# Kernel tuning notes

Measured on AMD Instinct MI355X. Metric: run time of the kernel, lower is better.

## Reference

```python
import jax, jax.numpy as jnp
import numpy as np

B, T, D = 4, 2048, 1024
H = int(D * 8.0)          # SwiGLU hidden (ffn_ratio=8)
SPARSITY = 0.95
THRESHOLD = 0.05          # PLIF firing threshold
PLIF_TAU = 2.5            # PLIF tau init
ALPHA = 2.0               # atan surrogate sharpness
EPS = 1e-6


@jax.custom_vjp
def spike(x):
    # Heaviside in fwd; atan surrogate gradient in bwd.
    return (x > 0).astype(x.dtype)

def _spike_fwd(x):
    return spike(x), x

def _spike_bwd(x, g):
    return (g * (ALPHA / 2.0) / (1.0 + (jnp.pi / 2.0 * ALPHA * x) ** 2),)

spike.defvjp(_spike_fwd, _spike_bwd)


def rmsnorm(x, w):
    return x * jax.lax.rsqrt(jnp.mean(x * x, axis=-1, keepdims=True) + EPS) * w


def setup_inputs() -> dict:
    key = jax.random.key(0)
    ks = jax.random.split(key, 12)
    f32 = jnp.float32
    return {
        "x": jax.random.normal(ks[0], (B, T, D), f32),
        "ln1_w": jnp.ones((D,), f32),
        "liq_win": (jax.random.normal(ks[1], (D, D), f32) / np.float32(np.sqrt(D))),
        "liq_wrec": (jax.random.normal(ks[2], (D, D), f32) / np.float32(np.sqrt(D))),
        "liq_b": jnp.zeros((D,), f32),
        "liq_tau": jnp.ones((D,), f32),  # softplus -> per-unit time constant
        "plif_w": jnp.asarray(-np.log(PLIF_TAU - 1.0), f32),  # sigmoid(w)=1/tau
        "syn_w": jax.random.normal(ks[3], (D, D), f32) * 0.02,
        "gate_w": jax.random.normal(ks[4], (D, D), f32) * 0.01,
        "gate_b": jnp.zeros((D,), f32),
        "ln2_w": jnp.ones((D,), f32),
        "ffn_wg": jax.random.normal(ks[5], (H, D), f32) * 0.02,
        "ffn_wu": jax.random.normal(ks[6], (H, D), f32) * 0.02,
        "ffn_wd": jax.random.normal(ks[7], (D, H), f32) * (0.02 / np.float32(np.sqrt(2.0))),
        "syn_mask": (jax.random.uniform(ks[8], (D, D)) > SPARSITY),  # bool, fixed
    }


def reference(x, ln1_w, liq_win, liq_wrec, liq_b, liq_tau, plif_w, syn_w,
              gate_w, gate_b, ln2_w, ffn_wg, ffn_wu, ffn_wd, syn_mask):
    # --- pre-norm ---
    a = rmsnorm(x, ln1_w)                       # (B,T,D)
    a_t = jnp.swapaxes(a, 0, 1)                 # (T,B,D)

    # --- LiquidCell: liquid time-constant recurrence over T ---
    tau = jax.nn.softplus(liq_tau)              # (D,) per-unit time constant

    def liq_step(h, xt):
        pre = xt @ liq_win.T + h @ liq_wrec.T + liq_b
        h = h + (jnp.tanh(pre) - h) / tau
        return h, h

    h0 = jnp.zeros((x.shape[0], D), x.dtype)
    _, h_seq = jax.lax.scan(liq_step, h0, a_t)  # (T,B,D)

    # --- PLIFCell.forward_seq: parametric LIF, subtract reset ---
    decay = jax.nn.sigmoid(plif_w)              # scalar = 1/tau_plif

    def plif_step(v, ht):
        v = v + decay * (ht - v)
        s = spike(v - THRESHOLD)
        v = v - s * THRESHOLD                   # reset='subtract'
        return v, s

    _, s_seq = jax.lax.scan(plif_step, jnp.zeros_like(h0), h_seq)
    s = jnp.swapaxes(s_seq, 0, 1)               # (B,T,D) spikes

    # --- SparseSynapse * sigmoid gate ---
    w_eff = syn_w * syn_mask.astype(syn_w.dtype)
    gated = (s @ w_eff.T) * jax.nn.sigmoid(s @ gate_w.T + gate_b)
    x = x + gated                               # dropout=0 -> identity

    # --- SwiGLU FFN residual ---
    y = rmsnorm(x, ln2_w)
    ff = (jax.nn.silu(y @ ffn_wg.T) * (y @ ffn_wu.T)) @ ffn_wd.T
    return x + ff
```

## Files before the change

### kernel.cpp

```cpp
#include <hip/hip_runtime.h>
#include <hip/hip_bf16.h>

#define TT 2048
#define DIM 1024
#define HFF 8192
#define NBATCH 4
#define PWG 32
#define THRESH 0.05f

typedef __bf16 bf16x8 __attribute__((ext_vector_type(8)));
typedef float f32x4 __attribute__((ext_vector_type(4)));

__device__ __forceinline__ unsigned short f2bf(float f) {
    __hip_bfloat16 h = __float2bfloat16(f);
    return __builtin_bit_cast(unsigned short, h);
}
__device__ __forceinline__ float bf2f(unsigned short u) {
    return __bfloat162float(__builtin_bit_cast(__hip_bfloat16, u));
}
__device__ __forceinline__ bf16x8 ldf(const unsigned short* p) {
    return *reinterpret_cast<const bf16x8*>(p);
}

__device__ __forceinline__ void ld2x4_mall(const float* p0, const float* p1,
                                           f32x4* a, f32x4* b) {
    asm volatile("global_load_dwordx4 %0, %2, off sc0 sc1\n\t"
                 "global_load_dwordx4 %1, %3, off sc0 sc1\n\t"
                 "s_waitcnt vmcnt(0)"
                 : "=&v"(*a), "=&v"(*b) : "v"(p0), "v"(p1) : "memory");
}

__global__ void maskprobe_k(const unsigned int* mask_words, int* flag) {
    __shared__ int allok;
    if (threadIdx.x == 0) allok = 1;
    __syncthreads();
    int ok = 1;
    for (int i = 0; i < 16; ++i) {
        unsigned int w = mask_words[threadIdx.x * 16 + i];
        if (w > 1u) ok = 0;
    }
    if (!ok) atomicAnd(&allok, 0);
    __syncthreads();
    if (threadIdx.x == 0) flag[0] = allok;
}

__global__ void weff_k(const float* __restrict__ synw, const void* __restrict__ mask,
                       const int* __restrict__ flag, unsigned short* __restrict__ dst) {
    const int isInt = flag[0];
    const int n = DIM * DIM;
    for (int i = blockIdx.x * 256 + threadIdx.x; i < n; i += gridDim.x * 256) {
        bool m;
        if (isInt) m = ((const int*)mask)[i] != 0;
        else       m = ((const unsigned char*)mask)[i] != 0;
        dst[i] = f2bf(m ? synw[i] : 0.f);
    }
}

__global__ void conv_k(const float* __restrict__ src, unsigned short* __restrict__ dst, int n) {
    for (int i = blockIdx.x * 256 + threadIdx.x; i < n; i += gridDim.x * 256)
        dst[i] = f2bf(src[i]);
}

__global__ void split_k(const float* __restrict__ src, unsigned short* __restrict__ hi,
                        unsigned short* __restrict__ lo, int n) {
    for (int i = blockIdx.x * 256 + threadIdx.x; i < n; i += gridDim.x * 256) {
        float v = src[i];
        unsigned short h = f2bf(v);
        hi[i] = h;
        lo[i] = f2bf(v - bf2f(h));
    }
}

__global__ void spkexp_k(const unsigned int* __restrict__ spk, unsigned short* __restrict__ sbf) {
    const int i = blockIdx.x * 256 + threadIdx.x;
    const unsigned int w = spk[i];
    const int d = i & 1023, t32 = (i >> 10) & 63, b = i >> 16;
    const size_t base = ((size_t)b * TT + (size_t)t32 * 32) * DIM + d;
    #pragma unroll
    for (int j = 0; j < 32; ++j)
        sbf[base + (size_t)j * DIM] = ((w >> j) & 1u) ? (unsigned short)0x3F80 : (unsigned short)0;
}

template <bool SPLIT>
__global__ void rms_k(const float* __restrict__ xin, const float* __restrict__ w,
                      unsigned short* __restrict__ hi, unsigned short* __restrict__ lo) {
    const int row = blockIdx.x;
    const int tid = threadIdx.x;
    const float4 xv = *reinterpret_cast<const float4*>(xin + (size_t)row * DIM + tid * 4);
    float ss = xv.x * xv.x + xv.y * xv.y + xv.z * xv.z + xv.w * xv.w;
    #pragma unroll
    for (int m = 1; m <= 32; m <<= 1) ss += __shfl_xor(ss, m);
    __shared__ float red[5];
    if ((tid & 63) == 0) red[tid >> 6] = ss;
    __syncthreads();
    if (tid == 0) {
        float s = red[0] + red[1] + red[2] + red[3];
        red[4] = 1.f / sqrtf(s * (1.f / DIM) + 1e-6f);
    }
    __syncthreads();
    const float scale = red[4];
    const float wv[4] = {w[tid*4], w[tid*4+1], w[tid*4+2], w[tid*4+3]};
    const float xa[4] = {xv.x, xv.y, xv.z, xv.w};
    #pragma unroll
    for (int i = 0; i < 4; ++i) {
        float v = xa[i] * scale * wv[i];
        unsigned short h = f2bf(v);
        hi[(size_t)row * DIM + tid * 4 + i] = h;
        if constexpr (SPLIT) lo[(size_t)row * DIM + tid * 4 + i] = f2bf(v - bf2f(h));
    }
}

template <int EPI>
__global__ __launch_bounds__(256, 1) void gemm_k(
    const unsigned short* __restrict__ A,  const unsigned short* __restrict__ Alo,
    const unsigned short* __restrict__ B1, const unsigned short* __restrict__ B1lo,
    const unsigned short* __restrict__ B2,
    const float* __restrict__ aux1, const float* __restrict__ aux2,
    float* __restrict__ outf, unsigned short* __restrict__ outbf,
    int M, int N, int K) {
    constexpr bool HILO = (EPI == 0);
    constexpr bool DUAL = (EPI == 1 || EPI == 2);
    const int lane = threadIdx.x & 63;
    const int wv = threadIdx.x >> 6;
    const int l15 = lane & 15, l4 = lane >> 4;
    const long row0 = (long)blockIdx.y * 128 + (wv >> 1) * 64;
    const long col0 = (long)blockIdx.x * 128 + (wv & 1) * 64;
    long aoff[4], boff[4];
    #pragma unroll
    for (int i = 0; i < 4; ++i) {
        aoff[i] = (row0 + i * 16 + l15) * (long)K + l4 * 8;
        boff[i] = (col0 + i * 16 + l15) * (long)K + l4 * 8;
    }
    f32x4 acc[4][4];
    f32x4 acc2[DUAL ? 4 : 1][DUAL ? 4 : 1];
    #pragma unroll
    for (int i = 0; i < 4; ++i)
        #pragma unroll
        for (int j = 0; j < 4; ++j) {
            acc[i][j] = (f32x4){0.f, 0.f, 0.f, 0.f};
            if constexpr (DUAL) acc2[i][j] = (f32x4){0.f, 0.f, 0.f, 0.f};
        }
    for (int kk = 0; kk < K; kk += 32) {
        bf16x8 af[4], bf_[4], al[4], bl[4], b2f[4];
        #pragma unroll
        for (int i = 0; i < 4; ++i) {
            af[i] = ldf(A + aoff[i] + kk);
            bf_[i] = ldf(B1 + boff[i] + kk);
            if constexpr (HILO) {
                al[i] = ldf(Alo + aoff[i] + kk);
                bl[i] = ldf(B1lo + boff[i] + kk);
            }
            if constexpr (DUAL) b2f[i] = ldf(B2 + boff[i] + kk);
        }
        #pragma unroll
        for (int i = 0; i < 4; ++i)
            #pragma unroll
            for (int j = 0; j < 4; ++j) {
                acc[i][j] = __builtin_amdgcn_mfma_f32_16x16x32_bf16(af[i], bf_[j], acc[i][j], 0, 0, 0);
                if constexpr (HILO) {
                    acc[i][j] = __builtin_amdgcn_mfma_f32_16x16x32_bf16(af[i], bl[j], acc[i][j], 0, 0, 0);
                    acc[i][j] = __builtin_amdgcn_mfma_f32_16x16x32_bf16(al[i], bf_[j], acc[i][j], 0, 0, 0);
                }
                if constexpr (DUAL)
                    acc2[i][j] = __builtin_amdgcn_mfma_f32_16x16x32_bf16(af[i], b2f[j], acc2[i][j], 0, 0, 0);
            }
    }
    #pragma unroll
    for (int i = 0; i < 4; ++i) {
        #pragma unroll
        for (int r = 0; r < 4; ++r) {
            const long row = row0 + i * 16 + l4 * 4 + r;
            #pragma unroll
            for (int j = 0; j < 4; ++j) {
                const long col = col0 + j * 16 + l15;
                float v = acc[i][j][r];
                if constexpr (EPI == 0) {
                    int m = (int)row;
                    int bb = m >> 11, tt = m & 2047;
                    outf[((size_t)(tt * NBATCH + bb)) * DIM + col] = v + aux1[col];
                } else if constexpr (EPI == 1) {
                    size_t idx = (size_t)row * N + col;
                    float gg = acc2[i][j][r] + aux2[col];
                    outf[idx] = aux1[idx] + v * (1.f / (1.f + expf(-gg)));
                } else if constexpr (EPI == 2) {
                    size_t idx = (size_t)row * N + col;
                    float u = acc2[i][j][r];
                    outbf[idx] = f2bf((v / (1.f + expf(-v))) * u);
                } else {
                    size_t idx = (size_t)row * N + col;
                    outf[idx] = aux1[idx] + v;
                }
            }
        }
    }
}

__global__ __launch_bounds__(512, 1) void recur_k(
    const float* __restrict__ wrec, const float* __restrict__ U,
    const float* __restrict__ liqtau, const float* __restrict__ plifw,
    float* __restrict__ hg, int* __restrict__ flags, unsigned int* __restrict__ spk) {
    const int tid = threadIdx.x;
    const int wg = blockIdx.x;
    const int g = tid >> 6;
    const int L = tid & 63;
    const int kp = L;
    const int d0 = wg * 32 + g * 4;

    float wreg[4][16];
    #pragma unroll
    for (int d = 0; d < 4; ++d) {
        const float* wr = wrec + (size_t)(d0 + d) * DIM + kp * 16;
        #pragma unroll
        for (int q = 0; q < 4; ++q) {
            f32x4 w4 = *reinterpret_cast<const f32x4*>(wr + q * 4);
            wreg[d][q*4+0] = w4[0]; wreg[d][q*4+1] = w4[1];
            wreg[d][q*4+2] = w4[2]; wreg[d][q*4+3] = w4[3];
        }
    }

    __shared__ float hl[4 * 1088];
    for (int i = tid; i < 4 * 1088; i += 512) hl[i] = 0.f;

    const int od = L >> 2, ob = L & 3;
    const int odim = d0 + od;
    const bool own = (L < 16);
    float hq = 0.f, vq = 0.f, tauv = 1.f;
    unsigned smask = 0u;
    const float decay = 1.f / (1.f + expf(-plifw[0]));
    if (own) {
        float lt = liqtau[odim];
        tauv = (lt > 20.f) ? lt : log1pf(expf(lt));
    }
    const int sel1 = L & 1, sel2 = (L >> 1) & 1, sel4 = (L >> 2) & 1, sel8 = (L >> 3) & 1;

    int cb[4];
    #pragma unroll
    for (int b = 0; b < 4; ++b)
        cb[b] = b * 1088 + (kp >> 2) * 68 + (kp & 3) * 16;
    __syncthreads();

    for (int t = 0; t < TT; ++t) {
        float uvp = 0.f;
        if (own) uvp = U[((size_t)t * NBATCH + ob) * DIM + odim];

        float a[16];
        #pragma unroll
        for (int v = 0; v < 16; ++v) a[v] = 0.f;
        #pragma unroll
        for (int q = 0; q < 4; ++q) {
            const f32x4 h0 = *reinterpret_cast<const f32x4*>(hl + cb[0] + q * 4);
            const f32x4 h1 = *reinterpret_cast<const f32x4*>(hl + cb[1] + q * 4);
            const f32x4 h2 = *reinterpret_cast<const f32x4*>(hl + cb[2] + q * 4);
            const f32x4 h3 = *reinterpret_cast<const f32x4*>(hl + cb[3] + q * 4);
            #pragma unroll
            for (int d = 0; d < 4; ++d)
                #pragma unroll
                for (int e = 0; e < 4; ++e) {
                    const float w = wreg[d][q * 4 + e];
                    a[d*4+0] = fmaf(w, h0[e], a[d*4+0]);
                    a[d*4+1] = fmaf(w, h1[e], a[d*4+1]);
                    a[d*4+2] = fmaf(w, h2[e], a[d*4+2]);
                    a[d*4+3] = fmaf(w, h3[e], a[d*4+3]);
                }
        }
        #pragma unroll
        for (int j = 0; j < 8; ++j) {
            float snd = sel1 ? a[2*j] : a[2*j+1];
            float kept = sel1 ? a[2*j+1] : a[2*j];
            a[j] = kept + __shfl_xor(snd, 1);
        }
        #pragma unroll
        for (int j = 0; j < 4; ++j) {
            float snd = sel2 ? a[2*j] : a[2*j+1];
            float kept = sel2 ? a[2*j+1] : a[2*j];
            a[j] = kept + __shfl_xor(snd, 2);
        }
        #pragma unroll
        for (int j = 0; j < 2; ++j) {
            float snd = sel4 ? a[2*j] : a[2*j+1];
            float kept = sel4 ? a[2*j+1] : a[2*j];
            a[j] = kept + __shfl_xor(snd, 4);
        }
        {
            float snd = sel8 ? a[0] : a[1];
            float kept = sel8 ? a[1] : a[0];
            a[0] = kept + __shfl_xor(snd, 8);
        }
        a[0] += __shfl_xor(a[0], 16);
        a[0] += __shfl_xor(a[0], 32);

        if (own) {
            float pre = a[0] + uvp;
            float th = tanhf(pre);
            float hn = hq + (th - hq) / tauv;
            hq = hn;
            float v = vq + decay * (hn - vq);
            float s = ((v - THRESH) > 0.f) ? 1.f : 0.f;
            vq = v - s * THRESH;
            smask |= (s > 0.f ? 1u : 0u) << (t & 31);
            if ((t & 31) == 31) {
                __hip_atomic_store(&spk[ob * 65536 + (t >> 5) * 1024 + odim], smask,
                                   __ATOMIC_RELAXED, __HIP_MEMORY_SCOPE_SYSTEM);
                smask = 0u;
            }
            __hip_atomic_store(&hg[(size_t)(t & 1) * 4096 + ob * 1024 + odim], hn,
                               __ATOMIC_RELAXED, __HIP_MEMORY_SCOPE_SYSTEM);
        }
        if (t == TT - 1) break;
        __syncthreads();
        if (tid == 0)
            __hip_atomic_store(&flags[wg], t + 1, __ATOMIC_RELAXED, __HIP_MEMORY_SCOPE_SYSTEM);
        if (g == 0) {
            while (__hip_atomic_load(&flags[L & 31], __ATOMIC_RELAXED,
                                     __HIP_MEMORY_SCOPE_SYSTEM) < t + 1) {}
        }
        __syncthreads();
        {
            const float* src = hg + (size_t)(t & 1) * 4096;
            const int b = tid >> 7, k0 = (tid & 127) * 8;
            const int w = b * 1088 + (k0 >> 6) * 68 + (k0 & 63);
            f32x4 va, vb;
            ld2x4_mall(src + b * 1024 + k0, src + b * 1024 + k0 + 4, &va, &vb);
            *reinterpret_cast<f32x4*>(hl + w) = va;
            *reinterpret_cast<f32x4*>(hl + w + 4) = vb;
        }
        __syncthreads();
    }
}

extern "C" void kernel_launch(void* const* d_in, const int* in_sizes, int n_in,
                              void* d_out, int out_size, void* d_ws, size_t ws_size,
                              hipStream_t stream) {
    (void)in_sizes; (void)n_in; (void)out_size; (void)ws_size;
    const float* x     = (const float*)d_in[0];
    const float* ln1   = (const float*)d_in[1];
    const float* win   = (const float*)d_in[2];
    const float* wrec  = (const float*)d_in[3];
    const float* liqb  = (const float*)d_in[4];
    const float* liqtau= (const float*)d_in[5];
    const float* plifw = (const float*)d_in[6];
    const float* synw  = (const float*)d_in[7];
    const float* gatew = (const float*)d_in[8];
    const float* gateb = (const float*)d_in[9];
    const float* ln2   = (const float*)d_in[10];
    const float* wgp   = (const float*)d_in[11];
    const float* wup   = (const float*)d_in[12];
    const float* wdp   = (const float*)d_in[13];
    const void*  mask  = d_in[14];
    float* dout = (float*)d_out;
    char* ws = (char*)d_ws;
    const size_t MB = (size_t)1 << 20;

    unsigned short* winh  = (unsigned short*)(ws + 0 * MB);
    unsigned short* winl  = (unsigned short*)(ws + 2 * MB);
    unsigned short* weffb = (unsigned short*)(ws + 4 * MB);
    unsigned short* gatewb= (unsigned short*)(ws + 6 * MB);
    unsigned short* wgb   = (unsigned short*)(ws + 8 * MB);
    unsigned short* wub   = (unsigned short*)(ws + 24 * MB);
    unsigned short* wdb   = (unsigned short*)(ws + 40 * MB);
    unsigned short* ahi   = (unsigned short*)(ws + 56 * MB);
    unsigned short* alo   = (unsigned short*)(ws + 72 * MB);
    float*          Ubuf  = (float*)(ws + 88 * MB);
    unsigned short* hffb  = (unsigned short*)(ws + 88 * MB);
    unsigned short* sbf   = (unsigned short*)(ws + 120 * MB);
    float*          x2    = (float*)(ws + 136 * MB);
    float*          hgb   = (float*)(ws + 168 * MB);
    int*            flags = (int*)(ws + 168 * MB + 64 * 1024);
    int*            flag  = (int*)(ws + 168 * MB + 80 * 1024);
    unsigned int*   spk   = (unsigned int*)(ws + 169 * MB);

    hipMemsetAsync(flags, 0, 512, stream);
    maskprobe_k<<<1, 256, 0, stream>>>((const unsigned int*)mask, flag);
    weff_k<<<1024, 256, 0, stream>>>(synw, mask, flag, weffb);
    split_k<<<1024, 256, 0, stream>>>(win, winh, winl, DIM * DIM);
    conv_k<<<1024, 256, 0, stream>>>(gatew, gatewb, DIM * DIM);
    conv_k<<<2048, 256, 0, stream>>>(wgp, wgb, HFF * DIM);
    conv_k<<<2048, 256, 0, stream>>>(wup, wub, HFF * DIM);
    conv_k<<<2048, 256, 0, stream>>>(wdp, wdb, DIM * HFF);

    rms_k<true><<<NBATCH * TT, 256, 0, stream>>>(x, ln1, ahi, alo);
    gemm_k<0><<<dim3(DIM / 128, (NBATCH * TT) / 128), 256, 0, stream>>>(
        ahi, alo, winh, winl, nullptr, liqb, nullptr, Ubuf, nullptr,
        NBATCH * TT, DIM, DIM);

    recur_k<<<PWG, 512, 0, stream>>>(wrec, Ubuf, liqtau, plifw, hgb, flags, spk);
    spkexp_k<<<(NBATCH * 64 * 1024) / 256, 256, 0, stream>>>(spk, sbf);

    gemm_k<1><<<dim3(DIM / 128, (NBATCH * TT) / 128), 256, 0, stream>>>(
        sbf, nullptr, weffb, nullptr, gatewb, x, gateb, x2, nullptr,
        NBATCH * TT, DIM, DIM);

    rms_k<false><<<NBATCH * TT, 256, 0, stream>>>(x2, ln2, ahi, nullptr);

    const int CH = 2048;
    for (int c = 0; c < (NBATCH * TT) / CH; ++c) {
        const size_t ro = (size_t)c * CH;
        gemm_k<2><<<dim3(HFF / 128, CH / 128), 256, 0, stream>>>(
            ahi + ro * DIM, nullptr, wgb, nullptr, wub, nullptr, nullptr,
            nullptr, hffb, CH, HFF, DIM);
        gemm_k<3><<<dim3(DIM / 128, CH / 128), 256, 0, stream>>>(
            hffb, nullptr, wdb, nullptr, nullptr, x2 + ro * DIM, nullptr,
            dout + ro * DIM, nullptr, CH, DIM, HFF);
    }
}
```

Measured before the change: 8.516 ms.

## Replace per-step workgroup barriers with per-wave flags in recurrence grid sync

The cross-workgroup handshake in the recurrent kernel now has each wave publish its own progress flag (32 WGs × 8 waves = 256 flags). Every wave polls all 256 flags directly with vector loads, replacing the two __syncthreads and the single-wave spin per timestep. This is meant to cut intra-block barrier latency on the serial 2048-step critical path. In exchange, polling traffic on the flags rises, and correctness now rests on each wave's own vmcnt wait ordering its h store before its flag store.

```diff
diff --git a/kernel.cpp b/kernel.cpp
--- a/kernel.cpp
+++ b/kernel.cpp
@@ -10,6 +10,7 @@
 
 typedef __bf16 bf16x8 __attribute__((ext_vector_type(8)));
 typedef float f32x4 __attribute__((ext_vector_type(4)));
+typedef int i32x4 __attribute__((ext_vector_type(4)));
 
 __device__ __forceinline__ unsigned short f2bf(float f) {
     __hip_bfloat16 h = __float2bfloat16(f);
@@ -28,6 +29,13 @@
                  "global_load_dwordx4 %1, %3, off sc0 sc1\n\t"
                  "s_waitcnt vmcnt(0)"
                  : "=&v"(*a), "=&v"(*b) : "v"(p0), "v"(p1) : "memory");
+}
+__device__ __forceinline__ i32x4 ld4_mall(const int* p) {
+    i32x4 v;
+    asm volatile("global_load_dwordx4 %0, %1, off sc0 sc1\n\t"
+                 "s_waitcnt vmcnt(0)"
+                 : "=&v"(v) : "v"(p) : "memory");
+    return v;
 }
 
 __global__ void maskprobe_k(const unsigned int* mask_words, int* flag) {
@@ -237,6 +245,10 @@
     #pragma unroll
     for (int b = 0; b < 4; ++b)
         cb[b] = b * 1088 + (kp >> 2) * 68 + (kp & 3) * 16;
+
+    const int rb = tid >> 7, rk0 = (tid & 127) * 8;
+    const int rw = rb * 1088 + (rk0 >> 6) * 68 + (rk0 & 63);
+    const int* fp = flags + L * 4;
     __syncthreads();
 
     for (int t = 0; t < TT; ++t) {
@@ -307,22 +319,22 @@
                                __ATOMIC_RELAXED, __HIP_MEMORY_SCOPE_SYSTEM);
         }
         if (t == TT - 1) break;
-        __syncthreads();
-        if (tid == 0)
-            __hip_atomic_store(&flags[wg], t + 1, __ATOMIC_RELAXED, __HIP_MEMORY_SCOPE_SYSTEM);
-        if (g == 0) {
-            while (__hip_atomic_load(&flags[L & 31], __ATOMIC_RELAXED,
-                                     __HIP_MEMORY_SCOPE_SYSTEM) < t + 1) {}
-        }
-        __syncthreads();
+        asm volatile("s_waitcnt vmcnt(0)" ::: "memory");
+        if (L == 0)
+            __hip_atomic_store(&flags[wg * 8 + g], t + 1,
+                               __ATOMIC_RELAXED, __HIP_MEMORY_SCOPE_SYSTEM);
+        while (true) {
+            i32x4 f = ld4_mall(fp);
+            bool ok = (f[0] >= t + 1) & (f[1] >= t + 1) &
+                      (f[2] >= t + 1) & (f[3] >= t + 1);
+            if (__all(ok)) break;
+        }
         {
             const float* src = hg + (size_t)(t & 1) * 4096;
-            const int b = tid >> 7, k0 = (tid & 127) * 8;
-            const int w = b * 1088 + (k0 >> 6) * 68 + (k0 & 63);
             f32x4 va, vb;
-            ld2x4_mall(src + b * 1024 + k0, src + b * 1024 + k0 + 4, &va, &vb);
-            *reinterpret_cast<f32x4*>(hl + w) = va;
-            *reinterpret_cast<f32x4*>(hl + w + 4) = vb;
+            ld2x4_mall(src + rb * 1024 + rk0, src + rb * 1024 + rk0 + 4, &va, &vb);
+            *reinterpret_cast<f32x4*>(hl + rw) = va;
+            *reinterpret_cast<f32x4*>(hl + rw + 4) = vb;
         }
         __syncthreads();
     }
@@ -369,7 +381,7 @@
     int*            flag  = (int*)(ws + 168 * MB + 80 * 1024);
     unsigned int*   spk   = (unsigned int*)(ws + 169 * MB);
 
-    hipMemsetAsync(flags, 0, 512, stream);
+    hipMemsetAsync(flags, 0, 1024, stream);
     maskprobe_k<<<1, 256, 0, stream>>>((const unsigned int*)mask, flag);
     weff_k<<<1024, 256, 0, stream>>>(synw, mask, flag, weffb);
     split_k<<<1024, 256, 0, stream>>>(win, winh, winl, DIM * DIM);
```

Result: slower. 18.61 ms (+118.5%).

## Add direct global-to-LDS loading GEMM for the SwiGLU FFN matmuls

Applied to the files above, without the earlier changes.

Adds a new gemm2_k kernel that stages 128x64 bf16 tiles of A and B straight from global memory into LDS with the global_load_lds builtin, bypassing registers, then runs 16x16x32 bf16 MFMAs from LDS. It replaces gemm_k for the FFN gate/up and down projections, which dominate the FLOPs. The LDS layout is unswizzled, so the fragment reads may hit bank conflicts. Loads are not double-buffered, so load latency is exposed between the two barriers on each K step.

```diff
diff --git a/kernel.cpp b/kernel.cpp
--- a/kernel.cpp
+++ b/kernel.cpp
@@ -28,6 +28,12 @@
                  "global_load_dwordx4 %1, %3, off sc0 sc1\n\t"
                  "s_waitcnt vmcnt(0)"
                  : "=&v"(*a), "=&v"(*b) : "v"(p0), "v"(p1) : "memory");
+}
+
+__device__ __forceinline__ void gload_lds16(const void* g, void* l) {
+    __builtin_amdgcn_global_load_lds(
+        (const __attribute__((address_space(1))) unsigned int*)g,
+        (__attribute__((address_space(3))) unsigned int*)l, 16, 0, 0);
 }
 
 __global__ void maskprobe_k(const unsigned int* mask_words, int* flag) {
@@ -188,6 +194,95 @@
                     outbf[idx] = f2bf((v / (1.f + expf(-v))) * u);
                 } else {
                     size_t idx = (size_t)row * N + col;
+                    outf[idx] = aux1[idx] + v;
+                }
+            }
+        }
+    }
+}
+
+template <int EPI>
+__global__ __launch_bounds__(256, 1) void gemm2_k(
+    const unsigned short* __restrict__ A,
+    const unsigned short* __restrict__ B1,
+    const unsigned short* __restrict__ B2,
+    const float* __restrict__ aux1,
+    float* __restrict__ outf, unsigned short* __restrict__ outbf,
+    int N, int K) {
+    constexpr bool DUAL = (EPI == 2);
+    __shared__ unsigned short sA[128 * 64];
+    __shared__ unsigned short sB1[128 * 64];
+    __shared__ unsigned short sB2[DUAL ? 128 * 64 : 8];
+    const int lane = threadIdx.x & 63;
+    const int wv = threadIdx.x >> 6;
+    const int l15 = lane & 15, l4 = lane >> 4;
+    const long row0 = (long)blockIdx.y * 128;
+    const long col0 = (long)blockIdx.x * 128;
+    const int wr = wv >> 1, wc = wv & 1;
+    const int crow = lane >> 3;
+    const int cbyte = (lane & 7) * 16;
+    f32x4 acc[4][4];
+    f32x4 acc2[DUAL ? 4 : 1][DUAL ? 4 : 1];
+    #pragma unroll
+    for (int i = 0; i < 4; ++i)
+        #pragma unroll
+        for (int j = 0; j < 4; ++j) {
+            acc[i][j] = (f32x4){0.f, 0.f, 0.f, 0.f};
+            if constexpr (DUAL) acc2[i][j] = (f32x4){0.f, 0.f, 0.f, 0.f};
+        }
+    for (int kt = 0; kt < K; kt += 64) {
+        #pragma unroll
+        for (int i = 0; i < 4; ++i) {
+            const int chunk = wv * 4 + i;
+            const int trow = chunk * 8 + crow;
+            const char* ga = (const char*)A +
+                ((row0 + trow) * (size_t)K + kt) * 2 + cbyte;
+            gload_lds16(ga, (char*)sA + chunk * 1024);
+            const char* gb1 = (const char*)B1 +
+                ((col0 + trow) * (size_t)K + kt) * 2 + cbyte;
+            gload_lds16(gb1, (char*)sB1 + chunk * 1024);
+            if constexpr (DUAL) {
+                const char* gb2 = (const char*)B2 +
+                    ((col0 + trow) * (size_t)K + kt) * 2 + cbyte;
+                gload_lds16(gb2, (char*)sB2 + chunk * 1024);
+            }
+        }
+        __syncthreads();
+        #pragma unroll
+        for (int kk2 = 0; kk2 < 64; kk2 += 32) {
+            bf16x8 af[4], bf_[4], b2f[4];
+            #pragma unroll
+            for (int i = 0; i < 4; ++i) {
+                af[i]  = ldf(sA  + (wr * 64 + i * 16 + l15) * 64 + kk2 + l4 * 8);
+                bf_[i] = ldf(sB1 + (wc * 64 + i * 16 + l15) * 64 + kk2 + l4 * 8);
+                if constexpr (DUAL)
+                    b2f[i] = ldf(sB2 + (wc * 64 + i * 16 + l15) * 64 + kk2 + l4 * 8);
+            }
+            #pragma unroll
+            for (int i = 0; i < 4; ++i)
+                #pragma unroll
+                for (int j = 0; j < 4; ++j) {
+                    acc[i][j] = __builtin_amdgcn_mfma_f32_16x16x32_bf16(af[i], bf_[j], acc[i][j], 0, 0, 0);
+                    if constexpr (DUAL)
+                        acc2[i][j] = __builtin_amdgcn_mfma_f32_16x16x32_bf16(af[i], b2f[j], acc2[i][j], 0, 0, 0);
+                }
+        }
+        __syncthreads();
+    }
+    #pragma unroll
+    for (int i = 0; i < 4; ++i) {
+        #pragma unroll
+        for (int r = 0; r < 4; ++r) {
+            const long row = row0 + wr * 64 + i * 16 + l4 * 4 + r;
+            #pragma unroll
+            for (int j = 0; j < 4; ++j) {
+                const long col = col0 + wc * 64 + j * 16 + l15;
+                float v = acc[i][j][r];
+                size_t idx = (size_t)row * N + col;
+                if constexpr (EPI == 2) {
+                    float u = acc2[i][j][r];
+                    outbf[idx] = f2bf((v / (1.f + expf(-v))) * u);
+                } else {
                     outf[idx] = aux1[idx] + v;
                 }
             }
@@ -395,11 +490,9 @@
     const int CH = 2048;
     for (int c = 0; c < (NBATCH * TT) / CH; ++c) {
         const size_t ro = (size_t)c * CH;
-        gemm_k<2><<<dim3(HFF / 128, CH / 128), 256, 0, stream>>>(
-            ahi + ro * DIM, nullptr, wgb, nullptr, wub, nullptr, nullptr,
-            nullptr, hffb, CH, HFF, DIM);
-        gemm_k<3><<<dim3(DIM / 128, CH / 128), 256, 0, stream>>>(
-            hffb, nullptr, wdb, nullptr, nullptr, x2 + ro * DIM, nullptr,
-            dout + ro * DIM, nullptr, CH, DIM, HFF);
-    }
-}
+        gemm2_k<2><<<dim3(HFF / 128, CH / 128), 256, 0, stream>>>(
+            ahi + ro * DIM, wgb, wub, nullptr, nullptr, hffb, HFF, DIM);
+        gemm2_k<3><<<dim3(DIM / 128, CH / 128), 256, 0, stream>>>(
+            hffb, wdb, nullptr, x2 + ro * DIM, dout + ro * DIM, nullptr, DIM, HFF);
+    }
+}
```

Measured after the change: 7.907 ms. 1.08x faster.

## Stage GEMM tiles through LDS with direct global-to-LDS loads

Applied to the files above, without the earlier changes.

The GEMM kernel now copies 128x64 A and B tiles into shared memory using global_load_lds, synchronises, and then feeds the MFMAs from LDS instead of having each wave load its fragments straight from global memory. Waves sharing rows or columns of the block tile stop fetching the same data redundantly, which cuts global/L2 traffic. The cost is two barriers per K-step with no double buffering, plus unswizzled LDS reads that may cause bank conflicts.

```diff
diff --git a/kernel.cpp b/kernel.cpp
--- a/kernel.cpp
+++ b/kernel.cpp
@@ -28,6 +28,12 @@
                  "global_load_dwordx4 %1, %3, off sc0 sc1\n\t"
                  "s_waitcnt vmcnt(0)"
                  : "=&v"(*a), "=&v"(*b) : "v"(p0), "v"(p1) : "memory");
+}
+
+__device__ __forceinline__ void gload_lds16(const void* g, void* l) {
+    __builtin_amdgcn_global_load_lds(
+        (const __attribute__((address_space(1))) unsigned int*)g,
+        (__attribute__((address_space(3))) unsigned int*)l, 16, 0, 0);
 }
 
 __global__ void maskprobe_k(const unsigned int* mask_words, int* flag) {
@@ -111,26 +117,28 @@
 }
 
 template <int EPI>
-__global__ __launch_bounds__(256, 1) void gemm_k(
+__global__ __launch_bounds__(256, 1) void gemm2_k(
     const unsigned short* __restrict__ A,  const unsigned short* __restrict__ Alo,
     const unsigned short* __restrict__ B1, const unsigned short* __restrict__ B1lo,
     const unsigned short* __restrict__ B2,
     const float* __restrict__ aux1, const float* __restrict__ aux2,
     float* __restrict__ outf, unsigned short* __restrict__ outbf,
-    int M, int N, int K) {
+    int N, int K) {
     constexpr bool HILO = (EPI == 0);
     constexpr bool DUAL = (EPI == 1 || EPI == 2);
+    __shared__ unsigned short sA[128 * 64];
+    __shared__ unsigned short sB1[128 * 64];
+    __shared__ unsigned short sAlo[HILO ? 128 * 64 : 8];
+    __shared__ unsigned short sBlo[HILO ? 128 * 64 : 8];
+    __shared__ unsigned short sB2[DUAL ? 128 * 64 : 8];
     const int lane = threadIdx.x & 63;
     const int wv = threadIdx.x >> 6;
     const int l15 = lane & 15, l4 = lane >> 4;
-    const long row0 = (long)blockIdx.y * 128 + (wv >> 1) * 64;
-    const long col0 = (long)blockIdx.x * 128 + (wv & 1) * 64;
-    long aoff[4], boff[4];
-    #pragma unroll
-    for (int i = 0; i < 4; ++i) {
-        aoff[i] = (row0 + i * 16 + l15) * (long)K + l4 * 8;
-        boff[i] = (col0 + i * 16 + l15) * (long)K + l4 * 8;
-    }
+    const long row0 = (long)blockIdx.y * 128;
+    const long col0 = (long)blockIdx.x * 128;
+    const int wr = wv >> 1, wc = wv & 1;
+    const int crow = lane >> 3;
+    const int cbyte = (lane & 7) * 16;
     f32x4 acc[4][4];
     f32x4 acc2[DUAL ? 4 : 1][DUAL ? 4 : 1];
     #pragma unroll
@@ -140,39 +148,58 @@
             acc[i][j] = (f32x4){0.f, 0.f, 0.f, 0.f};
             if constexpr (DUAL) acc2[i][j] = (f32x4){0.f, 0.f, 0.f, 0.f};
         }
-    for (int kk = 0; kk < K; kk += 32) {
-        bf16x8 af[4], bf_[4], al[4], bl[4], b2f[4];
+    for (int kt = 0; kt < K; kt += 64) {
         #pragma unroll
         for (int i = 0; i < 4; ++i) {
-            af[i] = ldf(A + aoff[i] + kk);
-            bf_[i] = ldf(B1 + boff[i] + kk);
+            const int chunk = wv * 4 + i;
+            const int trow = chunk * 8 + crow;
+            const size_t goffA = ((row0 + trow) * (size_t)K + kt) * 2 + cbyte;
+            const size_t goffB = ((col0 + trow) * (size_t)K + kt) * 2 + cbyte;
+            gload_lds16((const char*)A + goffA, (char*)sA + chunk * 1024);
+            gload_lds16((const char*)B1 + goffB, (char*)sB1 + chunk * 1024);
             if constexpr (HILO) {
-                al[i] = ldf(Alo + aoff[i] + kk);
-                bl[i] = ldf(B1lo + boff[i] + kk);
+                gload_lds16((const char*)Alo + goffA, (char*)sAlo + chunk * 1024);
+                gload_lds16((const char*)B1lo + goffB, (char*)sBlo + chunk * 1024);
             }
-            if constexpr (DUAL) b2f[i] = ldf(B2 + boff[i] + kk);
-        }
-        #pragma unroll
-        for (int i = 0; i < 4; ++i)
+            if constexpr (DUAL)
+                gload_lds16((const char*)B2 + goffB, (char*)sB2 + chunk * 1024);
+        }
+        __syncthreads();
+        #pragma unroll
+        for (int kk2 = 0; kk2 < 64; kk2 += 32) {
+            bf16x8 af[4], bf_[4], al[4], bl[4], b2f[4];
+            #pragma unroll
+            for (int i = 0; i < 4; ++i) {
+                const int ao = (wr * 64 + i * 16 + l15) * 64 + kk2 + l4 * 8;
+                const int bo = (wc * 64 + i * 16 + l15) * 64 + kk2 + l4 * 8;
+                af[i]  = ldf(sA + ao);
+                bf_[i] = ldf(sB1 + bo);
+                if constexpr (HILO) { al[i] = ldf(sAlo + ao); bl[i] = ldf(sBlo + bo); }
+                if constexpr (DUAL) b2f[i] = ldf(sB2 + bo);
+            }
+            #pragma unroll
+            for (int i = 0; i < 4; ++i)
+                #pragma unroll
+                for (int j = 0; j < 4; ++j) {
+                    acc[i][j] = __builtin_amdgcn_mfma_f32_16x16x32_bf16(af[i], bf_[j], acc[i][j], 0, 0, 0);
+                    if constexpr (HILO) {
+                        acc[i][j] = __builtin_amdgcn_mfma_f32_16x16x32_bf16(af[i], bl[j], acc[i][j], 0, 0, 0);
+                        acc[i][j] = __builtin_amdgcn_mfma_f32_16x16x32_bf16(al[i], bf_[j], acc[i][j], 0, 0, 0);
+                    }
+                    if constexpr (DUAL)
+                        acc2[i][j] = __builtin_amdgcn_mfma_f32_16x16x32_bf16(af[i], b2f[j], acc2[i][j], 0, 0, 0);
+                }
+        }
+        __syncthreads();
+    }
+    #pragma unroll
+    for (int i = 0; i < 4; ++i) {
+        #pragma unroll
+        for (int r = 0; r < 4; ++r) {
+            const long row = row0 + wr * 64 + i * 16 + l4 * 4 + r;
             #pragma unroll
             for (int j = 0; j < 4; ++j) {
-                acc[i][j] = __builtin_amdgcn_mfma_f32_16x16x32_bf16(af[i], bf_[j], acc[i][j], 0, 0, 0);
-                if constexpr (HILO) {
-                    acc[i][j] = __builtin_amdgcn_mfma_f32_16x16x32_bf16(af[i], bl[j], acc[i][j], 0, 0, 0);
-                    acc[i][j] = __builtin_amdgcn_mfma_f32_16x16x32_bf16(al[i], bf_[j], acc[i][j], 0, 0, 0);
-                }
-                if constexpr (DUAL)
-                    acc2[i][j] = __builtin_amdgcn_mfma_f32_16x16x32_bf16(af[i], b2f[j], acc2[i][j], 0, 0, 0);
-            }
-    }
-    #pragma unroll
-    for (int i = 0; i < 4; ++i) {
-        #pragma unroll
-        for (int r = 0; r < 4; ++r) {
-            const long row = row0 + i * 16 + l4 * 4 + r;
-            #pragma unroll
-            for (int j = 0; j < 4; ++j) {
-                const long col = col0 + j * 16 + l15;
+                const long col = col0 + wc * 64 + j * 16 + l15;
                 float v = acc[i][j][r];
                 if constexpr (EPI == 0) {
                     int m = (int)row;
@@ -379,27 +406,25 @@
     conv_k<<<2048, 256, 0, stream>>>(wdp, wdb, DIM * HFF);
 
     rms_k<true><<<NBATCH * TT, 256, 0, stream>>>(x, ln1, ahi, alo);
-    gemm_k<0><<<dim3(DIM / 128, (NBATCH * TT) / 128), 256, 0, stream>>>(
-        ahi, alo, winh, winl, nullptr, liqb, nullptr, Ubuf, nullptr,
-        NBATCH * TT, DIM, DIM);
+    gemm2_k<0><<<dim3(DIM / 128, (NBATCH * TT) / 128), 256, 0, stream>>>(
+        ahi, alo, winh, winl, nullptr, liqb, nullptr, Ubuf, nullptr, DIM, DIM);
 
     recur_k<<<PWG, 512, 0, stream>>>(wrec, Ubuf, liqtau, plifw, hgb, flags, spk);
     spkexp_k<<<(NBATCH * 64 * 1024) / 256, 256, 0, stream>>>(spk, sbf);
 
-    gemm_k<1><<<dim3(DIM / 128, (NBATCH * TT) / 128), 256, 0, stream>>>(
-        sbf, nullptr, weffb, nullptr, gatewb, x, gateb, x2, nullptr,
-        NBATCH * TT, DIM, DIM);
+    gemm2_k<1><<<dim3(DIM / 128, (NBATCH * TT) / 128), 256, 0, stream>>>(
+        sbf, nullptr, weffb, nullptr, gatewb, x, gateb, x2, nullptr, DIM, DIM);
 
     rms_k<false><<<NBATCH * TT, 256, 0, stream>>>(x2, ln2, ahi, nullptr);
 
     const int CH = 2048;
     for (int c = 0; c < (NBATCH * TT) / CH; ++c) {
         const size_t ro = (size_t)c * CH;
-        gemm_k<2><<<dim3(HFF / 128, CH / 128), 256, 0, stream>>>(
+        gemm2_k<2><<<dim3(HFF / 128, CH / 128), 256, 0, stream>>>(
             ahi + ro * DIM, nullptr, wgb, nullptr, wub, nullptr, nullptr,
-            nullptr, hffb, CH, HFF, DIM);
-        gemm_k<3><<<dim3(DIM / 128, CH / 128), 256, 0, stream>>>(
+            nullptr, hffb, HFF, DIM);
+        gemm2_k<3><<<dim3(DIM / 128, CH / 128), 256, 0, stream>>>(
             hffb, nullptr, wdb, nullptr, nullptr, x2 + ro * DIM, nullptr,
-            dout + ro * DIM, nullptr, CH, DIM, HFF);
-    }
-}
+            dout + ro * DIM, nullptr, DIM, HFF);
+    }
+}
```

After: 7.812 ms. 8.3% less time.
